# Kernel tuning notes

Measured on AMD Instinct MI355X. Metric: run time of the kernel, lower is better.

The kernel has to match this reference:

```python
import jax, jax.numpy as jnp
import numpy as np

N_NODES = 100000
N_EDGES = 1600000
N_GRAPHS = 512
F_IN = 64
H = 128
STEPS = 6


def setup_inputs() -> dict:
    key = jax.random.key(0)
    ks = jax.random.split(key, 10)
    x = jax.random.normal(ks[0], (N_NODES, F_IN), dtype=jnp.float32)
    edge_index = jax.random.randint(ks[1], (2, N_EDGES), 0, N_NODES, dtype=jnp.int64)
    batch = jnp.sort(jax.random.randint(ks[2], (N_NODES,), 0, N_GRAPHS, dtype=jnp.int64))
    s = 1.0 / np.sqrt(H)
    W_in = jax.random.uniform(ks[3], (F_IN, H), jnp.float32, -s, s)   # input_layer (no bias)
    W_mp = jax.random.uniform(ks[4], (STEPS, H, H), jnp.float32, -s, s)  # GatedGraphConv weight per step
    W_ih = jax.random.uniform(ks[5], (3 * H, H), jnp.float32, -s, s)  # GRUCell input weights (r,z,n)
    W_hh = jax.random.uniform(ks[6], (3 * H, H), jnp.float32, -s, s)
    b_ih = jax.random.uniform(ks[7], (3 * H,), jnp.float32, -s, s)
    b_hh = jax.random.uniform(ks[8], (3 * H,), jnp.float32, -s, s)
    W_p = jax.random.uniform(ks[9], (H, 1), jnp.float32, -s, s)       # prediction_layer
    b_p = jnp.zeros((1,), jnp.float32)
    return {"x": x, "edge_index": edge_index, "batch": batch, "W_in": W_in,
            "W_mp": W_mp, "W_ih": W_ih, "W_hh": W_hh, "b_ih": b_ih, "b_hh": b_hh,
            "W_p": W_p, "b_p": b_p}


def _gru_cell(m, h, W_ih, W_hh, b_ih, b_hh):
    # PyTorch GRUCell: gates ordered r, z, n
    gi = m @ W_ih.T + b_ih  # [N, 3H]
    gh = h @ W_hh.T + b_hh
    i_r, i_z, i_n = jnp.split(gi, 3, axis=-1)
    h_r, h_z, h_n = jnp.split(gh, 3, axis=-1)
    r = jax.nn.sigmoid(i_r + h_r)
    z = jax.nn.sigmoid(i_z + h_z)
    n = jnp.tanh(i_n + r * h_n)
    return (1.0 - z) * n + z * h


def reference(x, edge_index, batch, W_in, W_mp, W_ih, W_hh, b_ih, b_hh, W_p, b_p):
    src, dst = edge_index[0], edge_index[1]
    n_nodes = x.shape[0]

    h = jnp.tanh(x @ W_in)  # input_layer (no bias) + tanh -> [N, H]

    def step(h, W):
        m = h @ W                                    # per-step linear [N, H]
        agg = jax.ops.segment_sum(m[src], dst, num_segments=n_nodes)  # add-aggregation
        h = _gru_cell(agg, h, W_ih, W_hh, b_ih, b_hh)
        return h, None

    h, _ = jax.lax.scan(step, h, W_mp)

    # global_mean_pool over graphs
    sums = jax.ops.segment_sum(h, batch, num_segments=N_GRAPHS)       # [G, H]
    cnt = jax.ops.segment_sum(jnp.ones((n_nodes,), h.dtype), batch, num_segments=N_GRAPHS)
    pooled = sums / jnp.maximum(cnt, 1.0)[:, None]

    out = jax.nn.relu(pooled) @ W_p + b_p            # [G, 1]
    return out[:, 0]
```

## Files before the change

### kernel.cpp

```cpp
#include <hip/hip_runtime.h>

#define NN 100000
#define NE 1600000
#define NG 512
#define FIN 64
#define HD 128
#define NSTEP 6
#define SCHUNK 1024
#define NBLK 98

#define BROWS 128
#define NBUCK 782
#define EPER 16
#define BINBLK 391

typedef _Float16 f16x8 __attribute__((ext_vector_type(8)));
typedef _Float16 f16x4 __attribute__((ext_vector_type(4)));
typedef float    f32x4 __attribute__((ext_vector_type(4)));

__device__ __forceinline__ float sigm(float x) { return 1.f / (1.f + __expf(-x)); }
__device__ __forceinline__ float tanhfast(float x) { return 2.f / (1.f + __expf(-2.f * x)) - 1.f; }

__device__ __forceinline__ int lidx(int r, int col) {
    return r * 128 + ((((col >> 3) ^ (r & 15)) << 3) | (col & 7));
}

__global__ void k_count(const int* __restrict__ dst, int* __restrict__ counts) {
    int e = blockIdx.x * 256 + threadIdx.x;
    if (e < NE) atomicAdd(&counts[dst[e]], 1);
}

__global__ void k_scan1(const int* __restrict__ counts, int* __restrict__ indptr, int* __restrict__ aux) {
    __shared__ int sh[256];
    int blk = blockIdx.x, tid = threadIdx.x;
    int base = blk * SCHUNK + tid * 4;
    int v0 = 0, v1 = 0, v2 = 0, v3 = 0;
    if (base + 0 < NN) v0 = counts[base + 0];
    if (base + 1 < NN) v1 = counts[base + 1];
    if (base + 2 < NN) v2 = counts[base + 2];
    if (base + 3 < NN) v3 = counts[base + 3];
    int tsum = v0 + v1 + v2 + v3;
    sh[tid] = tsum;
    __syncthreads();
    for (int off = 1; off < 256; off <<= 1) {
        int t = (tid >= off) ? sh[tid - off] : 0;
        __syncthreads();
        sh[tid] += t;
        __syncthreads();
    }
    int excl = sh[tid] - tsum;
    if (base + 0 < NN) indptr[base + 0] = excl;
    if (base + 1 < NN) indptr[base + 1] = excl + v0;
    if (base + 2 < NN) indptr[base + 2] = excl + v0 + v1;
    if (base + 3 < NN) indptr[base + 3] = excl + v0 + v1 + v2;
    if (tid == 255) aux[blk] = sh[255];
}

__global__ void k_scan2(int* __restrict__ aux) {
    __shared__ int sh[128];
    int tid = threadIdx.x;
    int v = (tid < NBLK) ? aux[tid] : 0;
    sh[tid] = v;
    __syncthreads();
    for (int off = 1; off < 128; off <<= 1) {
        int t = (tid >= off) ? sh[tid - off] : 0;
        __syncthreads();
        sh[tid] += t;
        __syncthreads();
    }
    if (tid < NBLK) aux[tid] = sh[tid] - v;
}

__global__ void k_scan3(int* __restrict__ indptr, const int* __restrict__ aux) {
    int blk = blockIdx.x, tid = threadIdx.x;
    int off = aux[blk];
    int base = blk * SCHUNK + tid * 4;
#pragma unroll
    for (int i = 0; i < 4; ++i) {
        int idx = base + i;
        if (idx < NN) indptr[idx] += off;
    }
    if (blk == 0 && tid == 0) indptr[NN] = NE;
}


__global__ void k_bcinit(const int* __restrict__ indptr, int* __restrict__ bcur) {
    int b = blockIdx.x * 256 + threadIdx.x;
    if (b < NBUCK) bcur[b] = indptr[b * BROWS];
}

__global__ void __launch_bounds__(256) k_bin(const int* __restrict__ src, const int* __restrict__ dst,
                                             int* __restrict__ bcur, int2* __restrict__ pairs) {
    __shared__ int hist[NBUCK];
    __shared__ int base[NBUCK];
    int tid = threadIdx.x;
    for (int i = tid; i < NBUCK; i += 256) hist[i] = 0;
    __syncthreads();
    int e0 = blockIdx.x * (256 * EPER) + tid;
    int s[EPER], d[EPER], rk[EPER];
#pragma unroll
    for (int k = 0; k < EPER; ++k) {
        int e = e0 + k * 256;
        if (e < NE) {
            s[k] = src[e];
            d[k] = dst[e];
            rk[k] = atomicAdd(&hist[d[k] >> 7], 1);
        }
    }
    __syncthreads();
    for (int i = tid; i < NBUCK; i += 256) {
        int c = hist[i];
        base[i] = c ? atomicAdd(&bcur[i], c) : 0;
    }
    __syncthreads();
#pragma unroll
    for (int k = 0; k < EPER; ++k) {
        int e = e0 + k * 256;
        if (e < NE) pairs[base[d[k] >> 7] + rk[k]] = make_int2(s[k], d[k]);
    }
}

__global__ void __launch_bounds__(256) k_fill2(const int2* __restrict__ pairs,
                                               const int* __restrict__ indptr, int* __restrict__ csr) {
    __shared__ int cnt[BROWS];
    __shared__ int ip[BROWS];
    int b = blockIdx.x, tid = threadIdx.x;
    int n0 = b * BROWS;
    if (tid < BROWS) {
        cnt[tid] = 0;
        ip[tid] = (n0 + tid < NN) ? indptr[n0 + tid] : NE;
    }
    __syncthreads();
    int s = indptr[n0];
    int nend = n0 + BROWS; if (nend > NN) nend = NN;
    int e = indptr[nend];
    for (int i = s + tid; i < e; i += 256) {
        int2 p = pairs[i];
        int li = p.y & (BROWS - 1);
        int r = atomicAdd(&cnt[li], 1);
        csr[ip[li] + r] = p.x;
    }
}

__global__ void k_prepB(const float* __restrict__ Wmp, const float* __restrict__ Wih,
                        const float* __restrict__ Whh, _Float16* __restrict__ Bsw) {
    __shared__ float wih[HD];
    int b = blockIdx.x;
    int s = b >> 9;
    int c = b & 511;
    int g = c >> 7;
    int j = c & 127;
    int jj = (g < 2) ? c : (j + 256);
    int k = threadIdx.x;
    if (k < HD) wih[k] = Wih[(size_t)jj * HD + k];
    __syncthreads();
    float val = 0.f;
    if (k < 128) {
        if (g != 3) {
            const float* wm = Wmp + ((size_t)s * HD + k) * HD;
            float acc = 0.f;
#pragma unroll 8
            for (int t = 0; t < HD; ++t) acc += wm[t] * wih[t];
            val = acc;
        }
    } else {
        if (g != 2) val = Whh[(size_t)jj * HD + (k - 128)];
    }
    int l16 = c & 15, sub = (c >> 4) & 1, w = (c >> 5) & 3;
    int t = g * 2 + sub;
    int p = k >> 5, quad = (k >> 3) & 3, je = k & 7;
    size_t idx = (size_t)s * 131072 + ((size_t)((w * 8 + t) * 8 + p) * 64 + quad * 16 + l16) * 8 + je;
    Bsw[idx] = (_Float16)val;
}

__global__ void k_prepWin(const float* __restrict__ Win,
                          _Float16* __restrict__ BihW, _Float16* __restrict__ BilW) {
    int gid = blockIdx.x * 256 + threadIdx.x;
    int jj = gid & 7;
    int lane = (gid >> 3) & 63;
    int p = (gid >> 9) & 1;
    int t = (gid >> 10) & 7;
    int k = p * 32 + (lane >> 4) * 8 + jj;
    int col = t * 16 + (lane & 15);
    float val = Win[(size_t)k * HD + col];
    _Float16 hi = (_Float16)val;
    BihW[gid] = hi;
    BilW[gid] = (_Float16)(val - (float)hi);
}

__global__ void __launch_bounds__(256) k_input(const float* __restrict__ x,
                                               const _Float16* __restrict__ BihW,
                                               const _Float16* __restrict__ BilW,
                                               _Float16* __restrict__ H) {
    __shared__ _Float16 Xh[64 * 64];
    __shared__ _Float16 Xl[64 * 64];
    __shared__ _Float16 Oh[64 * 128];
    int tid = threadIdx.x;
    int w = tid >> 6, lane = tid & 63;
    int quad = lane >> 4, l16 = lane & 15;
    int m0 = blockIdx.x * 64;

#pragma unroll
    for (int it = 0; it < 4; ++it) {
        int c = it * 256 + tid;
        int row = c >> 4, cc = c & 15;
        int grow = m0 + row; if (grow >= NN) grow = NN - 1;
        float4 v = ((const float4*)(x + (size_t)grow * FIN))[cc];
        f16x4 vh, vl;
        vh[0] = (_Float16)v.x; vl[0] = (_Float16)(v.x - (float)vh[0]);
        vh[1] = (_Float16)v.y; vl[1] = (_Float16)(v.y - (float)vh[1]);
        vh[2] = (_Float16)v.z; vl[2] = (_Float16)(v.z - (float)vh[2]);
        vh[3] = (_Float16)v.w; vl[3] = (_Float16)(v.w - (float)vh[3]);
        int ld = row * 64 + ((((cc >> 1) ^ (row & 7)) << 3)) + (cc & 1) * 4;
        *(f16x4*)(&Xh[ld]) = vh;
        *(f16x4*)(&Xl[ld]) = vl;
    }
    __syncthreads();

    f32x4 acc[4][2];
#pragma unroll
    for (int mi = 0; mi < 4; ++mi) { acc[mi][0] = (f32x4){0,0,0,0}; acc[mi][1] = (f32x4){0,0,0,0}; }

#pragma unroll
    for (int p = 0; p < 2; ++p) {
        int ch = p * 4 + quad;
        f16x8 ah[4], al[4];
#pragma unroll
        for (int mi = 0; mi < 4; ++mi) {
            int r = mi * 16 + l16;
            int li = r * 64 + ((ch ^ (r & 7)) << 3);
            ah[mi] = *(const f16x8*)(&Xh[li]);
            al[mi] = *(const f16x8*)(&Xl[li]);
        }
#pragma unroll
        for (int t2 = 0; t2 < 2; ++t2) {
            int t = w * 2 + t2;
            f16x8 bh = *(const f16x8*)(BihW + ((size_t)(t * 2 + p) * 64 + lane) * 8);
            f16x8 blv = *(const f16x8*)(BilW + ((size_t)(t * 2 + p) * 64 + lane) * 8);
#pragma unroll
            for (int mi = 0; mi < 4; ++mi) {
                acc[mi][t2] = __builtin_amdgcn_mfma_f32_16x16x32_f16(ah[mi], bh, acc[mi][t2], 0, 0, 0);
                acc[mi][t2] = __builtin_amdgcn_mfma_f32_16x16x32_f16(ah[mi], blv, acc[mi][t2], 0, 0, 0);
                acc[mi][t2] = __builtin_amdgcn_mfma_f32_16x16x32_f16(al[mi], bh, acc[mi][t2], 0, 0, 0);
            }
        }
    }

#pragma unroll
    for (int t2 = 0; t2 < 2; ++t2) {
        int j = (w * 2 + t2) * 16 + l16;
#pragma unroll
        for (int mi = 0; mi < 4; ++mi) {
#pragma unroll
            for (int reg = 0; reg < 4; ++reg) {
                int row = mi * 16 + quad * 4 + reg;
                Oh[lidx(row, j)] = (_Float16)tanhfast(acc[mi][t2][reg]);
            }
        }
    }
    __syncthreads();
#pragma unroll
    for (int it = 0; it < 4; ++it) {
        int c = it * 256 + tid;
        int row = c >> 4, kc = c & 15;
        int grow = m0 + row;
        if (grow < NN) {
            int ld = row * 128 + ((kc ^ (row & 15)) << 3);
            *(f16x8*)(H + (size_t)grow * HD + kc * 8) = *(const f16x8*)(&Oh[ld]);
        }
    }
}

__global__ void k_agg(const _Float16* __restrict__ H, const int* __restrict__ indptr,
                      const int* __restrict__ csr, _Float16* __restrict__ Shi) {
    int v = blockIdx.x * 4 + (threadIdx.x >> 6);
    int lane = threadIdx.x & 63;
    int slot = lane >> 4;
    int cg = lane & 15;
    const _Float16* hp = H + cg * 8;
    int s = indptr[v], e = indptr[v + 1];
    float a0 = 0.f, a1 = 0.f, a2 = 0.f, a3 = 0.f, a4 = 0.f, a5 = 0.f, a6 = 0.f, a7 = 0.f;
    int i = s + slot;
    for (; i + 12 < e; i += 16) {
        int u0 = csr[i], u1 = csr[i + 4], u2 = csr[i + 8], u3 = csr[i + 12];
        f16x8 t0 = *(const f16x8*)(hp + (size_t)u0 * HD);
        f16x8 t1 = *(const f16x8*)(hp + (size_t)u1 * HD);
        f16x8 t2 = *(const f16x8*)(hp + (size_t)u2 * HD);
        f16x8 t3 = *(const f16x8*)(hp + (size_t)u3 * HD);
        a0 += (float)t0[0] + (float)t1[0] + (float)t2[0] + (float)t3[0];
        a1 += (float)t0[1] + (float)t1[1] + (float)t2[1] + (float)t3[1];
        a2 += (float)t0[2] + (float)t1[2] + (float)t2[2] + (float)t3[2];
        a3 += (float)t0[3] + (float)t1[3] + (float)t2[3] + (float)t3[3];
        a4 += (float)t0[4] + (float)t1[4] + (float)t2[4] + (float)t3[4];
        a5 += (float)t0[5] + (float)t1[5] + (float)t2[5] + (float)t3[5];
        a6 += (float)t0[6] + (float)t1[6] + (float)t2[6] + (float)t3[6];
        a7 += (float)t0[7] + (float)t1[7] + (float)t2[7] + (float)t3[7];
    }
    for (; i < e; i += 4) {
        int u0 = csr[i];
        f16x8 t0 = *(const f16x8*)(hp + (size_t)u0 * HD);
        a0 += (float)t0[0]; a1 += (float)t0[1]; a2 += (float)t0[2]; a3 += (float)t0[3];
        a4 += (float)t0[4]; a5 += (float)t0[5]; a6 += (float)t0[6]; a7 += (float)t0[7];
    }
    a0 += __shfl_down(a0, 32); a1 += __shfl_down(a1, 32);
    a2 += __shfl_down(a2, 32); a3 += __shfl_down(a3, 32);
    a4 += __shfl_down(a4, 32); a5 += __shfl_down(a5, 32);
    a6 += __shfl_down(a6, 32); a7 += __shfl_down(a7, 32);
    a0 += __shfl_down(a0, 16); a1 += __shfl_down(a1, 16);
    a2 += __shfl_down(a2, 16); a3 += __shfl_down(a3, 16);
    a4 += __shfl_down(a4, 16); a5 += __shfl_down(a5, 16);
    a6 += __shfl_down(a6, 16); a7 += __shfl_down(a7, 16);
    if (lane < 16) {
        f16x8 o;
        o[0] = (_Float16)a0; o[1] = (_Float16)a1; o[2] = (_Float16)a2; o[3] = (_Float16)a3;
        o[4] = (_Float16)a4; o[5] = (_Float16)a5; o[6] = (_Float16)a6; o[7] = (_Float16)a7;
        *(f16x8*)(Shi + (size_t)v * HD + cg * 8) = o;
    }
}

__global__ void __launch_bounds__(256, 3) k_ggemm(
        const _Float16* __restrict__ Shi, _Float16* __restrict__ H,
        const _Float16* __restrict__ Bsw,
        const float* __restrict__ bih, const float* __restrict__ bhh) {
    __shared__ _Float16 Sl[32 * 128];
    __shared__ _Float16 Hh[32 * 128];
    int tid = threadIdx.x;
    int w = tid >> 6, lane = tid & 63;
    int quad = lane >> 4, l16 = lane & 15;
    int m0 = blockIdx.x * 32;

    f16x8 hreg[2];
#pragma unroll
    for (int it = 0; it < 2; ++it) {
        int c = it * 256 + tid;
        int row = c >> 4, kc = c & 15;
        int grow = m0 + row;
        size_t gsrc = (size_t)grow * HD + kc * 8;
        int ld = row * 128 + ((kc ^ (row & 15)) << 3);
        *(f16x8*)(&Sl[ld]) = *(const f16x8*)(Shi + gsrc);
        hreg[it] = *(const f16x8*)(H + gsrc);
    }
    __syncthreads();

    f32x4 acc[2][8];
#pragma unroll
    for (int mi = 0; mi < 2; ++mi)
#pragma unroll
        for (int t = 0; t < 8; ++t) acc[mi][t] = (f32x4){0.f, 0.f, 0.f, 0.f};

    const _Float16* bw = Bsw + (size_t)(w * 8) * 8 * 512 + lane * 8;

#pragma unroll
    for (int p = 0; p < 4; ++p) {
        f16x8 a[2];
#pragma unroll
        for (int mi = 0; mi < 2; ++mi)
            a[mi] = *(const f16x8*)(&Sl[lidx(mi * 16 + l16, p * 32 + quad * 8)]);
#pragma unroll
        for (int t = 0; t < 6; ++t) {
            f16x8 b = *(const f16x8*)(bw + (size_t)(t * 8 + p) * 512);
#pragma unroll
            for (int mi = 0; mi < 2; ++mi)
                acc[mi][t] = __builtin_amdgcn_mfma_f32_16x16x32_f16(a[mi], b, acc[mi][t], 0, 0, 0);
        }
    }

#pragma unroll
    for (int it = 0; it < 2; ++it) {
        int c = it * 256 + tid;
        int row = c >> 4, kc = c & 15;
        int ld = row * 128 + ((kc ^ (row & 15)) << 3);
        *(f16x8*)(&Hh[ld]) = hreg[it];
    }
    __syncthreads();

#pragma unroll
    for (int p = 0; p < 4; ++p) {
        f16x8 a[2];
#pragma unroll
        for (int mi = 0; mi < 2; ++mi)
            a[mi] = *(const f16x8*)(&Hh[lidx(mi * 16 + l16, p * 32 + quad * 8)]);
#pragma unroll
        for (int tt = 0; tt < 6; ++tt) {
            int t = (tt < 4) ? tt : (tt + 2);
            f16x8 b = *(const f16x8*)(bw + (size_t)(t * 8 + p + 4) * 512);
#pragma unroll
            for (int mi = 0; mi < 2; ++mi)
                acc[mi][t] = __builtin_amdgcn_mfma_f32_16x16x32_f16(a[mi], b, acc[mi][t], 0, 0, 0);
        }
    }

    __syncthreads();

#pragma unroll
    for (int ns = 0; ns < 2; ++ns) {
        int j = w * 32 + ns * 16 + l16;
        float br  = bih[j]       + bhh[j];
        float bz  = bih[j + 128] + bhh[j + 128];
        float bin = bih[j + 256];
        float bhn = bhh[j + 256];
#pragma unroll
        for (int mi = 0; mi < 2; ++mi) {
#pragma unroll
            for (int reg = 0; reg < 4; ++reg) {
                int row = mi * 16 + quad * 4 + reg;
                int li = lidx(row, j);
                float hold = (float)Hh[li];
                float r = sigm(acc[mi][0 + ns][reg] + br);
                float z = sigm(acc[mi][2 + ns][reg] + bz);
                float n = tanhfast(acc[mi][4 + ns][reg] + bin + r * (acc[mi][6 + ns][reg] + bhn));
                Hh[li] = (_Float16)((1.f - z) * n + z * hold);
            }
        }
    }
    __syncthreads();

#pragma unroll
    for (int it = 0; it < 2; ++it) {
        int c = it * 256 + tid;
        int row = c >> 4, kc = c & 15;
        int grow = m0 + row;
        int ld = row * 128 + ((kc ^ (row & 15)) << 3);
        *(f16x8*)(H + (size_t)grow * HD + kc * 8) = *(const f16x8*)(&Hh[ld]);
    }
}

__global__ void k_ginit(int* __restrict__ gs, int* __restrict__ ge) {
    int g = threadIdx.x;
    if (g < NG) { gs[g] = 0; ge[g] = 0; }
}

__global__ void k_bounds(const int* __restrict__ batch, int* __restrict__ gs, int* __restrict__ ge) {
    int i = blockIdx.x * 256 + threadIdx.x;
    if (i >= NN) return;
    int b = batch[i];
    if (i == 0 || batch[i - 1] != b) gs[b] = i;
    if (i == NN - 1 || batch[i + 1] != b) ge[b] = i + 1;
}

__global__ void __launch_bounds__(256) k_pool(const _Float16* __restrict__ H,
                       const int* __restrict__ gs, const int* __restrict__ ge,
                       const float* __restrict__ Wp, const float* __restrict__ bp,
                       float* __restrict__ out) {
    __shared__ float red[4][HD];
    __shared__ float red2[HD];
    int g = blockIdx.x, tid = threadIdx.x;
    int w = tid >> 6, lane = tid & 63;
    int slot = tid >> 4;
    int cg = tid & 15;
    int s = gs[g], e = ge[g];
    float a0 = 0.f, a1 = 0.f, a2 = 0.f, a3 = 0.f, a4 = 0.f, a5 = 0.f, a6 = 0.f, a7 = 0.f;
    for (int n = s + slot; n < e; n += 16) {
        f16x8 v = *(const f16x8*)(H + (size_t)n * HD + cg * 8);
        a0 += (float)v[0]; a1 += (float)v[1]; a2 += (float)v[2]; a3 += (float)v[3];
        a4 += (float)v[4]; a5 += (float)v[5]; a6 += (float)v[6]; a7 += (float)v[7];
    }
    a0 += __shfl_down(a0, 32); a1 += __shfl_down(a1, 32);
    a2 += __shfl_down(a2, 32); a3 += __shfl_down(a3, 32);
    a4 += __shfl_down(a4, 32); a5 += __shfl_down(a5, 32);
    a6 += __shfl_down(a6, 32); a7 += __shfl_down(a7, 32);
    a0 += __shfl_down(a0, 16); a1 += __shfl_down(a1, 16);
    a2 += __shfl_down(a2, 16); a3 += __shfl_down(a3, 16);
    a4 += __shfl_down(a4, 16); a5 += __shfl_down(a5, 16);
    a6 += __shfl_down(a6, 16); a7 += __shfl_down(a7, 16);
    if (lane < 16) {
        red[w][cg * 8 + 0] = a0; red[w][cg * 8 + 1] = a1;
        red[w][cg * 8 + 2] = a2; red[w][cg * 8 + 3] = a3;
        red[w][cg * 8 + 4] = a4; red[w][cg * 8 + 5] = a5;
        red[w][cg * 8 + 6] = a6; red[w][cg * 8 + 7] = a7;
    }
    __syncthreads();
    if (tid < HD) {
        int cnt = e - s;
        float pooled = (red[0][tid] + red[1][tid] + red[2][tid] + red[3][tid])
                       / (float)(cnt > 0 ? cnt : 1);
        red2[tid] = fmaxf(pooled, 0.f) * Wp[tid];
    }
    __syncthreads();
    for (int off = 64; off > 0; off >>= 1) {
        if (tid < off) red2[tid] += red2[tid + off];
        __syncthreads();
    }
    if (tid == 0) out[g] = red2[0] + bp[0];
}

extern "C" void kernel_launch(void* const* d_in, const int* in_sizes, int n_in,
                              void* d_out, int out_size, void* d_ws, size_t ws_size,
                              hipStream_t stream) {
    const float* x   = (const float*)d_in[0];
    const int*   ei  = (const int*)d_in[1];
    const int*   bat = (const int*)d_in[2];
    const float* Win = (const float*)d_in[3];
    const float* Wmp = (const float*)d_in[4];
    const float* Wih = (const float*)d_in[5];
    const float* Whh = (const float*)d_in[6];
    const float* bih = (const float*)d_in[7];
    const float* bhh = (const float*)d_in[8];
    const float* Wp  = (const float*)d_in[9];
    const float* bp  = (const float*)d_in[10];
    float* out = (float*)d_out;

    const int* esrc = ei;
    const int* edst = ei + NE;

    char* w = (char*)d_ws;
    _Float16* H   = (_Float16*)w; w += (size_t)NN * HD * 2;
    _Float16* Shi = (_Float16*)w; w += (size_t)NN * HD * 2;
    _Float16* Bsw = (_Float16*)w; w += (size_t)NSTEP * 131072 * 2;
    _Float16* BihW = (_Float16*)w; w += 8192 * 2;
    _Float16* BilW = (_Float16*)w; w += 8192 * 2;
    int* indptr  = (int*)w;   w += 400128;
    int* cursor  = (int*)w;   w += 400128;
    int* csr     = (int*)w;   w += (size_t)NE * 4;
    int* aux     = (int*)w;   w += 512;
    int* gs      = (int*)w;   w += NG * 4;
    int* ge      = (int*)w;   w += NG * 4;

    int2* pairs = (int2*)Shi;
    int*  bcur  = cursor;

    hipMemsetAsync(cursor, 0, (size_t)NN * 4, stream);
    k_count<<<NE / 256, 256, 0, stream>>>(edst, cursor);
    k_scan1<<<NBLK, 256, 0, stream>>>(cursor, indptr, aux);
    k_scan2<<<1, 128, 0, stream>>>(aux);
    k_scan3<<<NBLK, 256, 0, stream>>>(indptr, aux);
    k_bcinit<<<(NBUCK + 255) / 256, 256, 0, stream>>>(indptr, bcur);
    k_bin<<<BINBLK, 256, 0, stream>>>(esrc, edst, bcur, pairs);
    k_fill2<<<NBUCK, 256, 0, stream>>>(pairs, indptr, csr);

    k_prepB<<<NSTEP * 512, 256, 0, stream>>>(Wmp, Wih, Whh, Bsw);
    k_prepWin<<<32, 256, 0, stream>>>(Win, BihW, BilW);
    k_input<<<(NN + 63) / 64, 256, 0, stream>>>(x, BihW, BilW, H);

    for (int st = 0; st < NSTEP; ++st) {
        k_agg<<<NN / 4, 256, 0, stream>>>(H, indptr, csr, Shi);
        k_ggemm<<<NN / 32, 256, 0, stream>>>(Shi, H,
                                             Bsw + (size_t)st * 131072,
                                             bih, bhh);
    }

    k_ginit<<<1, NG, 0, stream>>>(gs, ge);
    k_bounds<<<(NN + 255) / 256, 256, 0, stream>>>(bat, gs, ge);
    k_pool<<<NG, 256, 0, stream>>>(H, gs, ge, Wp, bp, out);
}
```

Baseline: 869.7 us.

## Build CSR via fixed-capacity buckets, dropping global degree count and scans

The separate global degree-count pass and its three-kernel prefix scan are removed. Edges are now binned straight into fixed-capacity per-bucket regions (3072 slots per 128-row bucket). A single-block scan over the bucket totals follows, and each fill block counts and scans its own rows' degrees in shared memory to write indptr and the CSR. This cuts 1.6M global atomics, a full read of dst and several launches, but it silently breaks if any bucket ever holds more than 3072 edges.

```diff
diff --git a/kernel.cpp b/kernel.cpp
--- a/kernel.cpp
+++ b/kernel.cpp
@@ -6,11 +6,10 @@
 #define FIN 64
 #define HD 128
 #define NSTEP 6
-#define SCHUNK 1024
-#define NBLK 98
 
 #define BROWS 128
 #define NBUCK 782
+#define BCAP 3072
 #define EPER 16
 #define BINBLK 391
 
@@ -25,69 +24,6 @@
     return r * 128 + ((((col >> 3) ^ (r & 15)) << 3) | (col & 7));
 }
 
-__global__ void k_count(const int* __restrict__ dst, int* __restrict__ counts) {
-    int e = blockIdx.x * 256 + threadIdx.x;
-    if (e < NE) atomicAdd(&counts[dst[e]], 1);
-}
-
-__global__ void k_scan1(const int* __restrict__ counts, int* __restrict__ indptr, int* __restrict__ aux) {
-    __shared__ int sh[256];
-    int blk = blockIdx.x, tid = threadIdx.x;
-    int base = blk * SCHUNK + tid * 4;
-    int v0 = 0, v1 = 0, v2 = 0, v3 = 0;
-    if (base + 0 < NN) v0 = counts[base + 0];
-    if (base + 1 < NN) v1 = counts[base + 1];
-    if (base + 2 < NN) v2 = counts[base + 2];
-    if (base + 3 < NN) v3 = counts[base + 3];
-    int tsum = v0 + v1 + v2 + v3;
-    sh[tid] = tsum;
-    __syncthreads();
-    for (int off = 1; off < 256; off <<= 1) {
-        int t = (tid >= off) ? sh[tid - off] : 0;
-        __syncthreads();
-        sh[tid] += t;
-        __syncthreads();
-    }
-    int excl = sh[tid] - tsum;
-    if (base + 0 < NN) indptr[base + 0] = excl;
-    if (base + 1 < NN) indptr[base + 1] = excl + v0;
-    if (base + 2 < NN) indptr[base + 2] = excl + v0 + v1;
-    if (base + 3 < NN) indptr[base + 3] = excl + v0 + v1 + v2;
-    if (tid == 255) aux[blk] = sh[255];
-}
-
-__global__ void k_scan2(int* __restrict__ aux) {
-    __shared__ int sh[128];
-    int tid = threadIdx.x;
-    int v = (tid < NBLK) ? aux[tid] : 0;
-    sh[tid] = v;
-    __syncthreads();
-    for (int off = 1; off < 128; off <<= 1) {
-        int t = (tid >= off) ? sh[tid - off] : 0;
-        __syncthreads();
-        sh[tid] += t;
-        __syncthreads();
-    }
-    if (tid < NBLK) aux[tid] = sh[tid] - v;
-}
-
-__global__ void k_scan3(int* __restrict__ indptr, const int* __restrict__ aux) {
-    int blk = blockIdx.x, tid = threadIdx.x;
-    int off = aux[blk];
-    int base = blk * SCHUNK + tid * 4;
-#pragma unroll
-    for (int i = 0; i < 4; ++i) {
-        int idx = base + i;
-        if (idx < NN) indptr[idx] += off;
-    }
-    if (blk == 0 && tid == 0) indptr[NN] = NE;
-}
-
-
-__global__ void k_bcinit(const int* __restrict__ indptr, int* __restrict__ bcur) {
-    int b = blockIdx.x * 256 + threadIdx.x;
-    if (b < NBUCK) bcur[b] = indptr[b * BROWS];
-}
 
 __global__ void __launch_bounds__(256) k_bin(const int* __restrict__ src, const int* __restrict__ dst,
                                              int* __restrict__ bcur, int2* __restrict__ pairs) {
@@ -116,26 +52,66 @@
 #pragma unroll
     for (int k = 0; k < EPER; ++k) {
         int e = e0 + k * 256;
-        if (e < NE) pairs[base[d[k] >> 7] + rk[k]] = make_int2(s[k], d[k]);
-    }
+        if (e < NE) {
+            int b = d[k] >> 7;
+            pairs[(size_t)b * BCAP + base[b] + rk[k]] = make_int2(s[k], d[k]);
+        }
+    }
+}
+
+__global__ void k_bscan(const int* __restrict__ bcnt, int* __restrict__ bbase) {
+    __shared__ int sh[1024];
+    int tid = threadIdx.x;
+    int v = (tid < NBUCK) ? bcnt[tid] : 0;
+    sh[tid] = v;
+    __syncthreads();
+    for (int off = 1; off < 1024; off <<= 1) {
+        int t = (tid >= off) ? sh[tid - off] : 0;
+        __syncthreads();
+        sh[tid] += t;
+        __syncthreads();
+    }
+    if (tid < NBUCK) bbase[tid] = sh[tid] - v;
+    if (tid == NBUCK - 1) bbase[NBUCK] = sh[tid];
 }
 
 __global__ void __launch_bounds__(256) k_fill2(const int2* __restrict__ pairs,
-                                               const int* __restrict__ indptr, int* __restrict__ csr) {
+                                               const int* __restrict__ bcnt,
+                                               const int* __restrict__ bbase,
+                                               int* __restrict__ indptr,
+                                               int* __restrict__ csr) {
     __shared__ int cnt[BROWS];
     __shared__ int ip[BROWS];
+    __shared__ int sc[BROWS];
     int b = blockIdx.x, tid = threadIdx.x;
     int n0 = b * BROWS;
+    if (tid < BROWS) cnt[tid] = 0;
+    __syncthreads();
+    int ec = bcnt[b];
+    const int2* pw = pairs + (size_t)b * BCAP;
+    for (int i = tid; i < ec; i += 256)
+        atomicAdd(&cnt[pw[i].y & (BROWS - 1)], 1);
+    __syncthreads();
+    if (tid < BROWS) sc[tid] = cnt[tid];
+    __syncthreads();
+    for (int off = 1; off < BROWS; off <<= 1) {
+        int t = (tid < BROWS && tid >= off) ? sc[tid - off] : 0;
+        __syncthreads();
+        if (tid < BROWS) sc[tid] += t;
+        __syncthreads();
+    }
+    int base = bbase[b];
     if (tid < BROWS) {
+        int v = base + sc[tid] - cnt[tid];
+        ip[tid] = v;
+        int n = n0 + tid;
+        if (n < NN) indptr[n] = v;
         cnt[tid] = 0;
-        ip[tid] = (n0 + tid < NN) ? indptr[n0 + tid] : NE;
-    }
-    __syncthreads();
-    int s = indptr[n0];
-    int nend = n0 + BROWS; if (nend > NN) nend = NN;
-    int e = indptr[nend];
-    for (int i = s + tid; i < e; i += 256) {
-        int2 p = pairs[i];
+    }
+    if (b == NBUCK - 1 && tid == 0) indptr[NN] = NE;
+    __syncthreads();
+    for (int i = tid; i < ec; i += 256) {
+        int2 p = pw[i];
         int li = p.y & (BROWS - 1);
         int r = atomicAdd(&cnt[li], 1);
         csr[ip[li] + r] = p.x;
@@ -510,23 +486,19 @@
     _Float16* BihW = (_Float16*)w; w += 8192 * 2;
     _Float16* BilW = (_Float16*)w; w += 8192 * 2;
     int* indptr  = (int*)w;   w += 400128;
-    int* cursor  = (int*)w;   w += 400128;
+    int* scratch = (int*)w;   w += 400128;
     int* csr     = (int*)w;   w += (size_t)NE * 4;
-    int* aux     = (int*)w;   w += 512;
     int* gs      = (int*)w;   w += NG * 4;
     int* ge      = (int*)w;   w += NG * 4;
 
+    int*  bcur  = scratch;
+    int*  bbase = scratch + 1024;
     int2* pairs = (int2*)Shi;
-    int*  bcur  = cursor;
-
-    hipMemsetAsync(cursor, 0, (size_t)NN * 4, stream);
-    k_count<<<NE / 256, 256, 0, stream>>>(edst, cursor);
-    k_scan1<<<NBLK, 256, 0, stream>>>(cursor, indptr, aux);
-    k_scan2<<<1, 128, 0, stream>>>(aux);
-    k_scan3<<<NBLK, 256, 0, stream>>>(indptr, aux);
-    k_bcinit<<<(NBUCK + 255) / 256, 256, 0, stream>>>(indptr, bcur);
+
+    hipMemsetAsync(bcur, 0, NBUCK * 4, stream);
     k_bin<<<BINBLK, 256, 0, stream>>>(esrc, edst, bcur, pairs);
-    k_fill2<<<NBUCK, 256, 0, stream>>>(pairs, indptr, csr);
+    k_bscan<<<1, 1024, 0, stream>>>(bcur, bbase);
+    k_fill2<<<NBUCK, 256, 0, stream>>>(pairs, bcur, bbase, indptr, csr);
 
     k_prepB<<<NSTEP * 512, 256, 0, stream>>>(Wmp, Wih, Whh, Bsw);
     k_prepWin<<<32, 256, 0, stream>>>(Win, BihW, BilW);
```

After: 803.9 us (median of 2 runs). 1.08x faster.
